# Kernel optimization log

Hardware: AMD Instinct MI355X
Metric: run time of the kernel (lower is better)

The kernel has to match this reference:

```python
import jax, jax.numpy as jnp
import numpy as np

D_MODEL = 2048
NUM_HEADS = 16
D_K = D_MODEL // NUM_HEADS


def setup_inputs() -> dict:
    key = jax.random.key(0)
    ks = jax.random.split(key, 12)
    B, S, D = 2, 2048, D_MODEL
    s = 1.0 / np.sqrt(D)
    return {
        "q": jax.random.normal(ks[0], (B, S, D), jnp.float32),
        "k": jax.random.normal(ks[1], (B, S, D), jnp.float32),
        "v": jax.random.normal(ks[2], (B, S, D), jnp.float32),
        "Wq": jax.random.normal(ks[3], (D, D), jnp.float32) * s,
        "bq": jax.random.normal(ks[4], (D,), jnp.float32) * 0.01,
        "Wk": jax.random.normal(ks[5], (D, D), jnp.float32) * s,
        "bk": jax.random.normal(ks[6], (D,), jnp.float32) * 0.01,
        "Wv": jax.random.normal(ks[7], (D, D), jnp.float32) * s,
        "bv": jax.random.normal(ks[8], (D,), jnp.float32) * 0.01,
        "Wo": jax.random.normal(ks[9], (D, D), jnp.float32) * s,
        "bo": jax.random.normal(ks[10], (D,), jnp.float32) * 0.01,
    }


def reference(q, k, v, Wq, bq, Wk, bk, Wv, bv, Wo, bo):
    B, S, D = q.shape
    H, dk = NUM_HEADS, D_K

    def proj(x, W, b):
        # Linear then split heads -> [B, H, S, dk]
        y = jnp.einsum('bsd,df->bsf', x, W) + b
        return y.reshape(B, -1, H, dk).transpose(0, 2, 1, 3)

    Q = proj(q, Wq, bq)
    K = proj(k, Wk, bk)
    V = proj(v, Wv, bv)

    scores = jnp.einsum('bhqd,bhkd->bhqk', Q, K) / jnp.sqrt(jnp.float32(dk))
    attn = jax.nn.softmax(scores, axis=-1)  # dropout is identity (eval)
    out = jnp.einsum('bhqk,bhkd->bhqd', attn, V)
    out = out.transpose(0, 2, 1, 3).reshape(B, -1, D)
    return jnp.einsum('bsd,df->bsf', out, Wo) + bo
```

## Files before the change

kernel.cpp:

```cpp
#include <hip/hip_runtime.h>
#include <hip/hip_bf16.h>
#include <stdint.h>

typedef float  f32x4  __attribute__((ext_vector_type(4)));
typedef float  f32x16 __attribute__((ext_vector_type(16)));
typedef short  s16x8  __attribute__((ext_vector_type(8)));

#define D_MODEL 2048
#define NHEADS  16
#define DK      128
#define BATCH   2
#define SEQ     2048
#define MROWS   (BATCH*SEQ)

__device__ __forceinline__ unsigned short f2bf(float f) {
  union { float f; unsigned int u; } v; v.f = f;
  unsigned int r = v.u + 0x7FFFu + ((v.u >> 16) & 1u);
  return (unsigned short)(r >> 16);
}

__device__ __forceinline__ unsigned int packbf(float lo, float hi) {
  return (unsigned int)f2bf(lo) | ((unsigned int)f2bf(hi) << 16);
}

__device__ __forceinline__ void async16(const void* g, void* l) {
  __builtin_amdgcn_global_load_lds(
      (const __attribute__((address_space(1))) unsigned int*)g,
      (__attribute__((address_space(3))) unsigned int*)l,
      16, 0, 0);
}

__global__ __launch_bounds__(256) void f2b3_kernel(const float* __restrict__ q,
                                                   const float* __restrict__ k,
                                                   const float* __restrict__ v,
                                                   unsigned short* __restrict__ qb,
                                                   unsigned short* __restrict__ kb,
                                                   unsigned short* __restrict__ vb) {
  const float* s; unsigned short* d;
  switch (blockIdx.y) {
    case 0:  s = q; d = qb; break;
    case 1:  s = k; d = kb; break;
    default: s = v; d = vb; break;
  }
  int i = blockIdx.x * 256 + threadIdx.x;
  const float4* s4 = (const float4*)s;
  float4 a = s4[2*i];
  float4 b = s4[2*i+1];
  s16x8 o;
  o[0] = (short)f2bf(a.x); o[1] = (short)f2bf(a.y);
  o[2] = (short)f2bf(a.z); o[3] = (short)f2bf(a.w);
  o[4] = (short)f2bf(b.x); o[5] = (short)f2bf(b.y);
  o[6] = (short)f2bf(b.z); o[7] = (short)f2bf(b.w);
  *(s16x8*)(d + 8*(size_t)i) = o;
}

__global__ __launch_bounds__(256) void wtrans_kernel(const float* __restrict__ Wq,
                                                     const float* __restrict__ Wk,
                                                     const float* __restrict__ Wv,
                                                     const float* __restrict__ Wo,
                                                     unsigned short* __restrict__ WqT,
                                                     unsigned short* __restrict__ WkT,
                                                     unsigned short* __restrict__ WvT,
                                                     unsigned short* __restrict__ WoT) {
  const float* W; unsigned short* Wt;
  switch (blockIdx.z) {
    case 0:  W = Wq; Wt = WqT; break;
    case 1:  W = Wk; Wt = WkT; break;
    case 2:  W = Wv; Wt = WvT; break;
    default: W = Wo; Wt = WoT; break;
  }
  __shared__ float tl[32][33];
  int x = threadIdx.x, y = threadIdx.y;
  int n0 = blockIdx.x * 32, k0 = blockIdx.y * 32;
  #pragma unroll
  for (int j = 0; j < 32; j += 8)
    tl[y + j][x] = W[(size_t)(k0 + y + j) * D_MODEL + n0 + x];
  __syncthreads();
  #pragma unroll
  for (int j = 0; j < 32; j += 8)
    Wt[(size_t)(n0 + y + j) * D_MODEL + k0 + x] = f2bf(tl[x][y + j]);
}

__global__ __launch_bounds__(256) void gemm_bt(const unsigned short* __restrict__ A,
                                               const unsigned short* __restrict__ Bt,
                                               const float* __restrict__ bias,
                                               void* __restrict__ Cout,
                                               int M, int N, int K,
                                               int mode, float scale) {
  __shared__ unsigned short As[128*32];
  __shared__ unsigned short Bs[128*32];
  const int t  = threadIdx.x;
  const int l  = t & 63, w = t >> 6;
  const int wr = w >> 1, wc = w & 1;
  const int m0 = blockIdx.y * 128, n0 = blockIdx.x * 128;
  const int lr = l & 15, lg = l >> 4;

  f32x4 acc[4][4] = {};

  for (int k0 = 0; k0 < K; k0 += 32) {
    __syncthreads();
    #pragma unroll
    for (int i = 0; i < 2; ++i) {
      int c    = t + 256*i;
      int row  = c >> 2;
      int col8 = (c & 3) * 8;
      async16(A  + (size_t)(m0 + row)*K + k0 + col8, (char*)As + c*16);
      async16(Bt + (size_t)(n0 + row)*K + k0 + col8, (char*)Bs + c*16);
    }
    asm volatile("s_waitcnt vmcnt(0)" ::: "memory");
    __syncthreads();

    s16x8 af[4], bfr[4];
    #pragma unroll
    for (int m = 0; m < 4; ++m)
      af[m] = *(const s16x8*)&As[(wr*64 + m*16 + lr)*32 + 8*lg];
    #pragma unroll
    for (int n = 0; n < 4; ++n)
      bfr[n] = *(const s16x8*)&Bs[(wc*64 + n*16 + lr)*32 + 8*lg];
    #pragma unroll
    for (int m = 0; m < 4; ++m)
      #pragma unroll
      for (int n = 0; n < 4; ++n)
        acc[m][n] = __builtin_amdgcn_mfma_f32_16x16x32_bf16(af[m], bfr[n], acc[m][n], 0, 0, 0);
  }

  if (mode == 0) {
    float* C = (float*)Cout;
    #pragma unroll
    for (int n = 0; n < 4; ++n) {
      int col = n0 + wc*64 + n*16 + lr;
      float bv = bias[col];
      #pragma unroll
      for (int m = 0; m < 4; ++m) {
        int rowb = m0 + wr*64 + m*16 + lg*4;
        #pragma unroll
        for (int r = 0; r < 4; ++r)
          C[(size_t)(rowb + r)*N + col] = (acc[m][n][r] + bv) * scale;
      }
    }
  } else {
    unsigned short* C = (unsigned short*)Cout;
    #pragma unroll
    for (int n = 0; n < 4; ++n) {
      int col = n0 + wc*64 + n*16 + lr;
      float bv = bias[col];
      int h = col >> 7, dkk = col & 127;
      #pragma unroll
      for (int m = 0; m < 4; ++m) {
        int rowb = m0 + wr*64 + m*16 + lg*4;
        #pragma unroll
        for (int r = 0; r < 4; ++r) {
          int row = rowb + r;
          int b = row >> 11, s = row & 2047;
          C[((size_t)((b*NHEADS + h)*SEQ + s))*DK + dkk] = f2bf((acc[m][n][r] + bv) * scale);
        }
      }
    }
  }
}

__global__ __launch_bounds__(256, 2) void attn_kernel(const unsigned short* __restrict__ Q,
                                                      const unsigned short* __restrict__ K,
                                                      const unsigned short* __restrict__ V,
                                                      unsigned short* __restrict__ O) {
  __shared__ char lds[64*256 + 128*144];
  unsigned short* Kl = (unsigned short*)lds;
  unsigned short* Vt = (unsigned short*)(lds + 64*256);

  const int t  = threadIdx.x;
  const int l  = t & 63, w = t >> 6;
  const int q_ = l & 31, hi = l >> 5;
  const int bh = blockIdx.y;
  const int b  = bh >> 4, h = bh & 15;
  const int q0 = blockIdx.x * 128;

  const unsigned short* Qp = Q + (size_t)bh * SEQ * DK;
  const unsigned short* Kp = K + (size_t)bh * SEQ * DK;
  const unsigned short* Vp = V + (size_t)bh * SEQ * DK;

  const int qrow = q0 + w*32 + q_;
  s16x8 aq[8];
  #pragma unroll
  for (int kk = 0; kk < 8; ++kk)
    aq[kk] = *(const s16x8*)(Qp + (size_t)qrow*DK + kk*16 + hi*8);

  f32x16 accO[4] = {};
  float m = -INFINITY, L = 0.f;

  const int vp_ = t & 31;
  const int vd0 = (t >> 5) * 8;

  for (int kv0 = 0; kv0 < SEQ; kv0 += 64) {
    __syncthreads();
    #pragma unroll
    for (int i = 0; i < 4; ++i) {
      int c   = t + 256*i;
      int row = c >> 4;
      int sb  = ((c & 15) << 4) ^ ((row & 15) << 4);
      async16((const char*)(Kp + (size_t)(kv0 + row)*DK) + sb, (char*)Kl + c*16);
    }
    #pragma unroll
    for (int rep = 0; rep < 2; ++rep) {
      int dvb = vd0 + rep*64;
      s16x8 va = *(const s16x8*)(Vp + (size_t)(kv0 + 2*vp_    )*DK + dvb);
      s16x8 vb = *(const s16x8*)(Vp + (size_t)(kv0 + 2*vp_ + 1)*DK + dvb);
      #pragma unroll
      for (int j = 0; j < 8; ++j) {
        unsigned int pk = (unsigned int)(unsigned short)va[j]
                        | ((unsigned int)(unsigned short)vb[j] << 16);
        *(unsigned int*)&Vt[(dvb + j)*72 + 2*vp_] = pk;
      }
    }
    asm volatile("s_waitcnt vmcnt(0) lgkmcnt(0)" ::: "memory");
    __syncthreads();

    f32x16 S0 = {}, S1 = {};
    #pragma unroll
    for (int t2 = 0; t2 < 2; ++t2) {
      int krow = t2*32 + q_;
      const char* kb = (const char*)Kl + krow*256;
      int swz = (krow & 15) << 4;
      #pragma unroll
      for (int kk = 0; kk < 8; ++kk) {
        s16x8 kf = *(const s16x8*)(kb + ((kk*32 + hi*16) ^ swz));
        if (t2 == 0) S0 = __builtin_amdgcn_mfma_f32_32x32x16_bf16(kf, aq[kk], S0, 0, 0, 0);
        else         S1 = __builtin_amdgcn_mfma_f32_32x32x16_bf16(kf, aq[kk], S1, 0, 0, 0);
      }
    }

    f32x16 mx;
    #pragma unroll
    for (int r = 0; r < 16; ++r) mx[r] = fmaxf(S0[r], S1[r]);
    float m8[8];
    #pragma unroll
    for (int r = 0; r < 8; ++r) m8[r] = fmaxf(mx[r], mx[r+8]);
    float m4a = fmaxf(m8[0], m8[4]), m4b = fmaxf(m8[1], m8[5]);
    float m4c = fmaxf(m8[2], m8[6]), m4d = fmaxf(m8[3], m8[7]);
    float pmax = fmaxf(fmaxf(m4a, m4b), fmaxf(m4c, m4d));
    pmax = fmaxf(pmax, __shfl_xor(pmax, 32, 64));
    float mnew = fmaxf(m, pmax);
    float corr = __expf(m - mnew);
    m = mnew;
    float rs0 = 0.f, rs1 = 0.f, rs2 = 0.f, rs3 = 0.f;
    #pragma unroll
    for (int r = 0; r < 4; ++r) {
      float a0 = __expf(S0[r]    - mnew); S0[r]    = a0; rs0 += a0;
      float a1 = __expf(S0[r+4]  - mnew); S0[r+4]  = a1; rs1 += a1;
      float a2 = __expf(S0[r+8]  - mnew); S0[r+8]  = a2; rs2 += a2;
      float a3 = __expf(S0[r+12] - mnew); S0[r+12] = a3; rs3 += a3;
      float b0 = __expf(S1[r]    - mnew); S1[r]    = b0; rs0 += b0;
      float b1 = __expf(S1[r+4]  - mnew); S1[r+4]  = b1; rs1 += b1;
      float b2 = __expf(S1[r+8]  - mnew); S1[r+8]  = b2; rs2 += b2;
      float b3 = __expf(S1[r+12] - mnew); S1[r+12] = b3; rs3 += b3;
    }
    float rs = (rs0 + rs1) + (rs2 + rs3);
    rs += __shfl_xor(rs, 32, 64);
    L = L*corr + rs;
    #pragma unroll
    for (int sub = 0; sub < 4; ++sub)
      #pragma unroll
      for (int r = 0; r < 16; ++r) accO[sub][r] *= corr;

    s16x8 PB[4];
    #pragma unroll
    for (int t2 = 0; t2 < 2; ++t2) {
      #pragma unroll
      for (int half = 0; half < 2; ++half) {
        int bse = half*8;
        unsigned int pkA01, pkA23, pkB01, pkB23;
        if (t2 == 0) {
          pkA01 = packbf(S0[bse+0], S0[bse+1]);
          pkA23 = packbf(S0[bse+2], S0[bse+3]);
          pkB01 = packbf(S0[bse+4], S0[bse+5]);
          pkB23 = packbf(S0[bse+6], S0[bse+7]);
        } else {
          pkA01 = packbf(S1[bse+0], S1[bse+1]);
          pkA23 = packbf(S1[bse+2], S1[bse+3]);
          pkB01 = packbf(S1[bse+4], S1[bse+5]);
          pkB23 = packbf(S1[bse+6], S1[bse+7]);
        }
        unsigned int xA01 = __shfl_xor(pkA01, 32, 64);
        unsigned int xA23 = __shfl_xor(pkA23, 32, 64);
        unsigned int xB01 = __shfl_xor(pkB01, 32, 64);
        unsigned int xB23 = __shfl_xor(pkB23, 32, 64);
        union { unsigned int u[4]; s16x8 v; } f;
        f.u[0] = hi ? xB01 : pkA01;
        f.u[1] = hi ? xB23 : pkA23;
        f.u[2] = hi ? pkB01 : xA01;
        f.u[3] = hi ? pkB23 : xA23;
        PB[t2*2 + half] = f.v;
      }
    }

    #pragma unroll
    for (int sub = 0; sub < 4; ++sub) {
      const char* vb2 = (const char*)Vt + (size_t)(sub*32 + q_)*144 + hi*16;
      #pragma unroll
      for (int kk = 0; kk < 4; ++kk) {
        s16x8 vf = *(const s16x8*)(vb2 + kk*32);
        accO[sub] = __builtin_amdgcn_mfma_f32_32x32x16_bf16(vf, PB[kk], accO[sub], 0, 0, 0);
      }
    }
  }

  __syncthreads();
  unsigned short* Ob = (unsigned short*)lds + (size_t)w*4096;
  float inv = 1.0f / L;
  #pragma unroll
  for (int sub = 0; sub < 4; ++sub)
    #pragma unroll
    for (int j = 0; j < 8; ++j) {
      unsigned int pw = packbf(accO[sub][2*j]*inv, accO[sub][2*j+1]*inv);
      int dv = sub*32 + (j&1)*2 + ((j>>1)*8) + 4*hi;
      *(unsigned int*)((char*)Ob + q_*256 + ((dv*2) ^ ((q_ & 15) << 4))) = pw;
    }
  asm volatile("s_waitcnt lgkmcnt(0)" ::: "memory");
  size_t gbase = ((size_t)(b*SEQ + q0 + w*32 + q_))*D_MODEL + h*DK;
  #pragma unroll
  for (int p = 0; p < 8; ++p) {
    int chunk = hi + 2*p;
    s16x8 ov = *(const s16x8*)((char*)Ob + q_*256 + ((chunk*16) ^ ((q_ & 15) << 4)));
    *(s16x8*)(O + gbase + chunk*8) = ov;
  }
}

extern "C" void kernel_launch(void* const* d_in, const int* in_sizes, int n_in,
                              void* d_out, int out_size, void* d_ws, size_t ws_size,
                              hipStream_t stream) {
  const float* q  = (const float*)d_in[0];
  const float* k  = (const float*)d_in[1];
  const float* v  = (const float*)d_in[2];
  const float* Wq = (const float*)d_in[3];
  const float* bq = (const float*)d_in[4];
  const float* Wk = (const float*)d_in[5];
  const float* bk = (const float*)d_in[6];
  const float* Wv = (const float*)d_in[7];
  const float* bv = (const float*)d_in[8];
  const float* Wo = (const float*)d_in[9];
  const float* bo = (const float*)d_in[10];
  float* out = (float*)d_out;

  char* ws = (char*)d_ws;
  const size_t SZT = (size_t)MROWS * D_MODEL * 2;
  const size_t SZW = (size_t)D_MODEL * D_MODEL * 2;

  unsigned short* qb  = (unsigned short*)(ws);
  unsigned short* kb  = (unsigned short*)(ws + SZT);
  unsigned short* vb  = (unsigned short*)(ws + 2*SZT);
  unsigned short* WqT = (unsigned short*)(ws + 3*SZT);
  unsigned short* WkT = (unsigned short*)(ws + 3*SZT + SZW);
  unsigned short* WvT = (unsigned short*)(ws + 3*SZT + 2*SZW);
  unsigned short* WoT = (unsigned short*)(ws + 3*SZT + 3*SZW);
  unsigned short* Qh  = (unsigned short*)(ws + 3*SZT + 4*SZW);
  unsigned short* Kh  = (unsigned short*)(ws + 4*SZT + 4*SZW);
  unsigned short* Vh  = (unsigned short*)(ws + 5*SZT + 4*SZW);
  unsigned short* Oc  = qb;

  const int n8 = MROWS * D_MODEL / 8;
  f2b3_kernel<<<dim3(n8/256, 3), 256, 0, stream>>>(q, k, v, qb, kb, vb);
  wtrans_kernel<<<dim3(64, 64, 4), dim3(32, 8), 0, stream>>>(Wq, Wk, Wv, Wo, WqT, WkT, WvT, WoT);

  const float qscale = 0.08838834764831845f;
  gemm_bt<<<dim3(16, 32), 256, 0, stream>>>(qb, WqT, bq, Qh, MROWS, D_MODEL, D_MODEL, 1, qscale);
  gemm_bt<<<dim3(16, 32), 256, 0, stream>>>(kb, WkT, bk, Kh, MROWS, D_MODEL, D_MODEL, 1, 1.0f);
  gemm_bt<<<dim3(16, 32), 256, 0, stream>>>(vb, WvT, bv, Vh, MROWS, D_MODEL, D_MODEL, 1, 1.0f);

  attn_kernel<<<dim3(SEQ/128, BATCH*NHEADS), 256, 0, stream>>>(Qh, Kh, Vh, Oc);

  gemm_bt<<<dim3(16, 32), 256, 0, stream>>>(Oc, WoT, bo, out, MROWS, D_MODEL, D_MODEL, 0, 1.0f);
}
```

Before: 368.1 us.

## Double-buffer K/V tiles in attention, use exp2 with lazy rescaling

The attention kernel now double-buffers LDS so the K async loads and V register loads for the next tile are issued before computing the current one, overlapping global memory with MFMA work. The softmax switches to exp2f by folding log2(e) into the Q scale. It also skips the running-max update and accumulator rescale unless some lane's max grows by more than 11. bf16 packing uses the library conversion. LDS doubles to about 69 KB per block, which could reduce occupancy below the 2 blocks per CU requested by launch bounds. The lazy rescale lets exponents reach up to 2^11, which bounds fp32/bf16 range risk.

```diff
diff --git a/kernel.cpp b/kernel.cpp
--- a/kernel.cpp
+++ b/kernel.cpp
@@ -21,6 +21,15 @@
 
 __device__ __forceinline__ unsigned int packbf(float lo, float hi) {
   return (unsigned int)f2bf(lo) | ((unsigned int)f2bf(hi) << 16);
+}
+
+__device__ __forceinline__ unsigned int packbf_c(float lo, float hi) {
+  __hip_bfloat16 l = __float2bfloat16(lo);
+  __hip_bfloat16 h = __float2bfloat16(hi);
+  unsigned short lu, hu;
+  __builtin_memcpy(&lu, &l, 2);
+  __builtin_memcpy(&hu, &h, 2);
+  return (unsigned int)lu | ((unsigned int)hu << 16);
 }
 
 __device__ __forceinline__ void async16(const void* g, void* l) {
@@ -163,9 +172,8 @@
                                                       const unsigned short* __restrict__ K,
                                                       const unsigned short* __restrict__ V,
                                                       unsigned short* __restrict__ O) {
-  __shared__ char lds[64*256 + 128*144];
-  unsigned short* Kl = (unsigned short*)lds;
-  unsigned short* Vt = (unsigned short*)(lds + 64*256);
+  #define BUFSZ (64*256 + 128*144)
+  __shared__ char lds[2*BUFSZ];
 
   const int t  = threadIdx.x;
   const int l  = t & 63, w = t >> 6;
@@ -190,35 +198,61 @@
   const int vp_ = t & 31;
   const int vd0 = (t >> 5) * 8;
 
-  for (int kv0 = 0; kv0 < SEQ; kv0 += 64) {
-    __syncthreads();
+  s16x8 va0, vb0, va1, vb1;
+
+  {
+    char* KlN = lds;
     #pragma unroll
     for (int i = 0; i < 4; ++i) {
       int c   = t + 256*i;
       int row = c >> 4;
       int sb  = ((c & 15) << 4) ^ ((row & 15) << 4);
-      async16((const char*)(Kp + (size_t)(kv0 + row)*DK) + sb, (char*)Kl + c*16);
-    }
-    #pragma unroll
-    for (int rep = 0; rep < 2; ++rep) {
-      int dvb = vd0 + rep*64;
-      s16x8 va = *(const s16x8*)(Vp + (size_t)(kv0 + 2*vp_    )*DK + dvb);
-      s16x8 vb = *(const s16x8*)(Vp + (size_t)(kv0 + 2*vp_ + 1)*DK + dvb);
-      #pragma unroll
-      for (int j = 0; j < 8; ++j) {
-        unsigned int pk = (unsigned int)(unsigned short)va[j]
-                        | ((unsigned int)(unsigned short)vb[j] << 16);
-        *(unsigned int*)&Vt[(dvb + j)*72 + 2*vp_] = pk;
-      }
-    }
-    asm volatile("s_waitcnt vmcnt(0) lgkmcnt(0)" ::: "memory");
+      async16((const char*)(Kp + (size_t)row*DK) + sb, KlN + c*16);
+    }
+    va0 = *(const s16x8*)(Vp + (size_t)(2*vp_    )*DK + vd0);
+    vb0 = *(const s16x8*)(Vp + (size_t)(2*vp_ + 1)*DK + vd0);
+    va1 = *(const s16x8*)(Vp + (size_t)(2*vp_    )*DK + vd0 + 64);
+    vb1 = *(const s16x8*)(Vp + (size_t)(2*vp_ + 1)*DK + vd0 + 64);
+  }
+
+  for (int tt = 0; tt < SEQ/64; ++tt) {
+    char*           Kl = lds + (tt & 1)*BUFSZ;
+    unsigned short* Vt = (unsigned short*)(Kl + 64*256);
+
+    asm volatile("s_waitcnt vmcnt(0)" ::: "memory");
+    #pragma unroll
+    for (int j = 0; j < 8; ++j) {
+      unsigned int pk0 = (unsigned int)(unsigned short)va0[j]
+                       | ((unsigned int)(unsigned short)vb0[j] << 16);
+      *(unsigned int*)&Vt[(vd0 + j)*72 + 2*vp_] = pk0;
+      unsigned int pk1 = (unsigned int)(unsigned short)va1[j]
+                       | ((unsigned int)(unsigned short)vb1[j] << 16);
+      *(unsigned int*)&Vt[(vd0 + 64 + j)*72 + 2*vp_] = pk1;
+    }
+    asm volatile("s_waitcnt lgkmcnt(0)" ::: "memory");
     __syncthreads();
+
+    if (tt + 1 < SEQ/64) {
+      int   kvn = (tt + 1) * 64;
+      char* KlN = lds + ((tt & 1) ^ 1)*BUFSZ;
+      #pragma unroll
+      for (int i = 0; i < 4; ++i) {
+        int c   = t + 256*i;
+        int row = c >> 4;
+        int sb  = ((c & 15) << 4) ^ ((row & 15) << 4);
+        async16((const char*)(Kp + (size_t)(kvn + row)*DK) + sb, KlN + c*16);
+      }
+      va0 = *(const s16x8*)(Vp + (size_t)(kvn + 2*vp_    )*DK + vd0);
+      vb0 = *(const s16x8*)(Vp + (size_t)(kvn + 2*vp_ + 1)*DK + vd0);
+      va1 = *(const s16x8*)(Vp + (size_t)(kvn + 2*vp_    )*DK + vd0 + 64);
+      vb1 = *(const s16x8*)(Vp + (size_t)(kvn + 2*vp_ + 1)*DK + vd0 + 64);
+    }
 
     f32x16 S0 = {}, S1 = {};
     #pragma unroll
     for (int t2 = 0; t2 < 2; ++t2) {
       int krow = t2*32 + q_;
-      const char* kb = (const char*)Kl + krow*256;
+      const char* kb = Kl + krow*256;
       int swz = (krow & 15) << 4;
       #pragma unroll
       for (int kk = 0; kk < 8; ++kk) {
@@ -231,35 +265,40 @@
     f32x16 mx;
     #pragma unroll
     for (int r = 0; r < 16; ++r) mx[r] = fmaxf(S0[r], S1[r]);
-    float m8[8];
-    #pragma unroll
-    for (int r = 0; r < 8; ++r) m8[r] = fmaxf(mx[r], mx[r+8]);
-    float m4a = fmaxf(m8[0], m8[4]), m4b = fmaxf(m8[1], m8[5]);
-    float m4c = fmaxf(m8[2], m8[6]), m4d = fmaxf(m8[3], m8[7]);
+    float m8_[8];
+    #pragma unroll
+    for (int r = 0; r < 8; ++r) m8_[r] = fmaxf(mx[r], mx[r+8]);
+    float m4a = fmaxf(m8_[0], m8_[4]), m4b = fmaxf(m8_[1], m8_[5]);
+    float m4c = fmaxf(m8_[2], m8_[6]), m4d = fmaxf(m8_[3], m8_[7]);
     float pmax = fmaxf(fmaxf(m4a, m4b), fmaxf(m4c, m4d));
     pmax = fmaxf(pmax, __shfl_xor(pmax, 32, 64));
-    float mnew = fmaxf(m, pmax);
-    float corr = __expf(m - mnew);
-    m = mnew;
+
+    if (!__all(pmax <= m + 11.0f)) {
+      float mnew = fmaxf(m, pmax);
+      float corr = exp2f(m - mnew);
+      m = mnew;
+      L *= corr;
+      #pragma unroll
+      for (int sub = 0; sub < 4; ++sub)
+        #pragma unroll
+        for (int r = 0; r < 16; ++r) accO[sub][r] *= corr;
+    }
+
     float rs0 = 0.f, rs1 = 0.f, rs2 = 0.f, rs3 = 0.f;
     #pragma unroll
     for (int r = 0; r < 4; ++r) {
-      float a0 = __expf(S0[r]    - mnew); S0[r]    = a0; rs0 += a0;
-      float a1 = __expf(S0[r+4]  - mnew); S0[r+4]  = a1; rs1 += a1;
-      float a2 = __expf(S0[r+8]  - mnew); S0[r+8]  = a2; rs2 += a2;
-      float a3 = __expf(S0[r+12] - mnew); S0[r+12] = a3; rs3 += a3;
-      float b0 = __expf(S1[r]    - mnew); S1[r]    = b0; rs0 += b0;
-      float b1 = __expf(S1[r+4]  - mnew); S1[r+4]  = b1; rs1 += b1;
-      float b2 = __expf(S1[r+8]  - mnew); S1[r+8]  = b2; rs2 += b2;
-      float b3 = __expf(S1[r+12] - mnew); S1[r+12] = b3; rs3 += b3;
+      float a0 = exp2f(S0[r]    - m); S0[r]    = a0; rs0 += a0;
+      float a1 = exp2f(S0[r+4]  - m); S0[r+4]  = a1; rs1 += a1;
+      float a2 = exp2f(S0[r+8]  - m); S0[r+8]  = a2; rs2 += a2;
+      float a3 = exp2f(S0[r+12] - m); S0[r+12] = a3; rs3 += a3;
+      float b0 = exp2f(S1[r]    - m); S1[r]    = b0; rs0 += b0;
+      float b1 = exp2f(S1[r+4]  - m); S1[r+4]  = b1; rs1 += b1;
+      float b2 = exp2f(S1[r+8]  - m); S1[r+8]  = b2; rs2 += b2;
+      float b3 = exp2f(S1[r+12] - m); S1[r+12] = b3; rs3 += b3;
     }
     float rs = (rs0 + rs1) + (rs2 + rs3);
     rs += __shfl_xor(rs, 32, 64);
-    L = L*corr + rs;
-    #pragma unroll
-    for (int sub = 0; sub < 4; ++sub)
-      #pragma unroll
-      for (int r = 0; r < 16; ++r) accO[sub][r] *= corr;
+    L += rs;
 
     s16x8 PB[4];
     #pragma unroll
@@ -269,15 +308,15 @@
         int bse = half*8;
         unsigned int pkA01, pkA23, pkB01, pkB23;
         if (t2 == 0) {
-          pkA01 = packbf(S0[bse+0], S0[bse+1]);
-          pkA23 = packbf(S0[bse+2], S0[bse+3]);
-          pkB01 = packbf(S0[bse+4], S0[bse+5]);
-          pkB23 = packbf(S0[bse+6], S0[bse+7]);
+          pkA01 = packbf_c(S0[bse+0], S0[bse+1]);
+          pkA23 = packbf_c(S0[bse+2], S0[bse+3]);
+          pkB01 = packbf_c(S0[bse+4], S0[bse+5]);
+          pkB23 = packbf_c(S0[bse+6], S0[bse+7]);
         } else {
-          pkA01 = packbf(S1[bse+0], S1[bse+1]);
-          pkA23 = packbf(S1[bse+2], S1[bse+3]);
-          pkB01 = packbf(S1[bse+4], S1[bse+5]);
-          pkB23 = packbf(S1[bse+6], S1[bse+7]);
+          pkA01 = packbf_c(S1[bse+0], S1[bse+1]);
+          pkA23 = packbf_c(S1[bse+2], S1[bse+3]);
+          pkB01 = packbf_c(S1[bse+4], S1[bse+5]);
+          pkB23 = packbf_c(S1[bse+6], S1[bse+7]);
         }
         unsigned int xA01 = __shfl_xor(pkA01, 32, 64);
         unsigned int xA23 = __shfl_xor(pkA23, 32, 64);
@@ -310,7 +349,7 @@
   for (int sub = 0; sub < 4; ++sub)
     #pragma unroll
     for (int j = 0; j < 8; ++j) {
-      unsigned int pw = packbf(accO[sub][2*j]*inv, accO[sub][2*j+1]*inv);
+      unsigned int pw = packbf_c(accO[sub][2*j]*inv, accO[sub][2*j+1]*inv);
       int dv = sub*32 + (j&1)*2 + ((j>>1)*8) + 4*hi;
       *(unsigned int*)((char*)Ob + q_*256 + ((dv*2) ^ ((q_ & 15) << 4))) = pw;
     }
@@ -322,6 +361,7 @@
     s16x8 ov = *(const s16x8*)((char*)Ob + q_*256 + ((chunk*16) ^ ((q_ & 15) << 4)));
     *(s16x8*)(O + gbase + chunk*8) = ov;
   }
+  #undef BUFSZ
 }
 
 extern "C" void kernel_launch(void* const* d_in, const int* in_sizes, int n_in,
@@ -360,7 +400,7 @@
   f2b3_kernel<<<dim3(n8/256, 3), 256, 0, stream>>>(q, k, v, qb, kb, vb);
   wtrans_kernel<<<dim3(64, 64, 4), dim3(32, 8), 0, stream>>>(Wq, Wk, Wv, Wo, WqT, WkT, WvT, WoT);
 
-  const float qscale = 0.08838834764831845f;
+  const float qscale = 0.1275174308f;
   gemm_bt<<<dim3(16, 32), 256, 0, stream>>>(qb, WqT, bq, Qh, MROWS, D_MODEL, D_MODEL, 1, qscale);
   gemm_bt<<<dim3(16, 32), 256, 0, stream>>>(kb, WkT, bk, Kh, MROWS, D_MODEL, D_MODEL, 1, 1.0f);
   gemm_bt<<<dim3(16, 32), 256, 0, stream>>>(vb, WvT, bv, Vh, MROWS, D_MODEL, D_MODEL, 1, 1.0f);
```

Result: no change. 374.5 us (+1.7%).
